# Kernel tuning notes

Measured on AMD Instinct MI355X. Metric: run time of the kernel, lower is better.

Reference implementation:

```python
import jax, jax.numpy as jnp
import numpy as np

BETA = 1.0

def setup_inputs() -> dict:
    key = jax.random.key(0)
    k1, k2 = jax.random.split(key)
    z = jax.random.normal(k1, (8, 8192, 64), dtype=jnp.float32)
    # codebook initialized as randn * sc (sc=0.001) in the original module
    codebook = jax.random.normal(k2, (1024, 64), dtype=jnp.float32) * 0.001
    return {"z": z, "codebook": codebook}

def reference(z, codebook):
    # squared euclidean distances: ||z||^2 + ||c||^2 - 2 z.c  -> [B, T, code_num]
    d = (jnp.sum(z ** 2, axis=-1, keepdims=True)
         + jnp.sum(codebook ** 2, axis=1)
         - 2.0 * jnp.einsum('btd,kd->btk', z, codebook))
    min_encoding_indices = jnp.argmin(d, axis=-1)            # [B, T] int
    # one-hot @ codebook is exactly a gather of nearest code vectors
    z_q = codebook[min_encoding_indices]                     # [B, T, D]
    sg = jax.lax.stop_gradient
    loss = jnp.mean((sg(z_q) - z) ** 2) + BETA * jnp.mean((z_q - sg(z)) ** 2)
    # straight-through estimator
    z_q_st = z + sg(z_q - z)
    return (z_q_st, min_encoding_indices, loss)
```

## Files before the change

### kernel.cpp

```cpp
#include <hip/hip_runtime.h>

#define TOKENS 65536
#define DIM 64
#define NCODE 1024
#define MARGIN 6e-5f
#define FLAG_CAP 8192
#define TPG 16

#define OUT_IDX_OFF ((size_t)TOKENS * DIM)
#define OUT_LOSS_OFF (OUT_IDX_OFF + TOKENS)

#define WS_LOSS   0
#define WS_FLAGC  8
#define WS_DONEA  12
#define WS_DGRP   16
#define WS_BNORM  2064
#define WS_CHI    6160
#define WS_CLO    137232
#define WS_PACKED 268304
#define WS_FLAGS  333840

typedef __attribute__((ext_vector_type(8))) short short8;
typedef __attribute__((ext_vector_type(4))) float f32x4;

__device__ __forceinline__ float np_sumsq64(const float* __restrict__ x) {
#pragma clang fp contract(off)
    float r[8];
#pragma unroll
    for (int j = 0; j < 8; ++j) r[j] = x[j] * x[j];
#pragma unroll
    for (int i = 8; i < 64; i += 8) {
#pragma unroll
        for (int j = 0; j < 8; ++j) {
            float sq = x[i + j] * x[i + j];
            r[j] = r[j] + sq;
        }
    }
    return ((r[0] + r[1]) + (r[2] + r[3])) + ((r[4] + r[5]) + (r[6] + r[7]));
}

__global__ __launch_bounds__(256) void vq_prep(
    const float* __restrict__ cb, unsigned short* __restrict__ chi,
    unsigned short* __restrict__ clo, float* __restrict__ bnorm,
    unsigned int* __restrict__ ctrl ) {
    int tid = blockIdx.x * 256 + threadIdx.x;
    if (tid < 516) ctrl[tid] = 0u;
    int j = tid & 7;
    int L = (tid >> 3) & 63;
    int cs = tid >> 9;
    int s = cs & 1, c = cs >> 1;
    int code = c * 16 + (L & 15);
    int d = s * 32 + (L >> 4) * 8 + j;
    float v = -2.0f * cb[(size_t)code * DIM + d];
    unsigned int b = __float_as_uint(v);
    chi[tid] = (unsigned short)(b >> 16);
    float hf = __uint_as_float(b & 0xFFFF0000u);
    float lo;
    {
#pragma clang fp contract(off)
        lo = v - hf;
    }
    clo[tid] = (unsigned short)(__float_as_uint(lo) >> 16);

    if (tid < NCODE) bnorm[tid] = np_sumsq64(cb + (size_t)tid * DIM);
}

__device__ __forceinline__ void top2_merge(float& a1, float& a2, int& ai,
                                           float b1, float b2, int bi) {
    float n1 = fminf(a1, b1);
    float n2 = fminf(fmaxf(a1, b1), fminf(a2, b2));
    ai = (b1 < a1) ? bi : ai;
    a1 = n1; a2 = n2;
}

__global__ __launch_bounds__(256, 4) void vq_fast(
    const float* __restrict__ z, const float* __restrict__ cb,
    const unsigned short* __restrict__ cfrag_hi,
    const unsigned short* __restrict__ cfrag_lo,
    const float* __restrict__ bnorm, float* __restrict__ out,
    unsigned int* __restrict__ flag_count, int* __restrict__ flag_list,
    unsigned long long* __restrict__ packed_min,
    double* __restrict__ loss_sum, unsigned int flag_cap) {
    __shared__ short8 sh_hi[2][512];
    __shared__ short8 sh_lo[2][512];
    __shared__ float bn_lds[NCODE];
    __shared__ int s_best[64];
    __shared__ int s_flag[64];

    const int tid = threadIdx.x;
    const int lane = tid & 63;
    const int w = tid >> 6;
    const int t0 = blockIdx.x * 64;
    const int tw = t0 + w * 16;
    const int col = lane & 15;
    const int quad = lane >> 4;

    ((float4*)bn_lds)[tid] = ((const float4*)bnorm)[tid];

    short8 zhi[2], zlo[2];
#pragma unroll
    for (int s = 0; s < 2; ++s) {
        const float* zp = z + (size_t)(tw + col) * DIM + s * 32 + quad * 8;
        float4 f0 = ((const float4*)zp)[0];
        float4 f1 = ((const float4*)zp)[1];
        float f[8] = {f0.x, f0.y, f0.z, f0.w, f1.x, f1.y, f1.z, f1.w};
        short8 h, l;
#pragma unroll
        for (int j = 0; j < 8; ++j) {
            unsigned int b = __float_as_uint(f[j]);
            h[j] = (short)(b >> 16);
            float hf = __uint_as_float(b & 0xFFFF0000u);
            float lo;
            {
#pragma clang fp contract(off)
                lo = f[j] - hf;
            }
            l[j] = (short)(__float_as_uint(lo) >> 16);
        }
        zhi[s] = h; zlo[s] = l;
    }

    const short8* CH = (const short8*)cfrag_hi;
    const short8* CL = (const short8*)cfrag_lo;

    {
        short8 a0 = CH[tid], a1 = CH[tid + 256];
        short8 b0 = CL[tid], b1 = CL[tid + 256];
        sh_hi[0][tid] = a0; sh_hi[0][tid + 256] = a1;
        sh_lo[0][tid] = b0; sh_lo[0][tid + 256] = b1;
    }
    __syncthreads();

    float m1 = 3.0e38f, m2 = 3.0e38f;
    int bi = 0;
    const int koff = quad * 4;

    for (int g = 0; g < 16; ++g) {
        const int buf = g & 1;
        short8 a0, a1, b0, b1;
        if (g < 15) {
            const int base = (g + 1) * 512 + tid;
            a0 = CH[base]; a1 = CH[base + 256];
            b0 = CL[base]; b1 = CL[base + 256];
        }
#pragma unroll
        for (int cc = 0; cc < 4; ++cc) {
            const int c = g * 4 + cc;
            short8 ch0 = sh_hi[buf][(cc * 2 + 0) * 64 + lane];
            short8 ch1 = sh_hi[buf][(cc * 2 + 1) * 64 + lane];
            short8 cl0 = sh_lo[buf][(cc * 2 + 0) * 64 + lane];
            short8 cl1 = sh_lo[buf][(cc * 2 + 1) * 64 + lane];
            const int cbase = c * 16 + koff;
            const f32x4 bn = *(const f32x4*)&bn_lds[cbase];
            f32x4 acc = bn;
            acc = __builtin_amdgcn_mfma_f32_16x16x32_bf16(ch0, zhi[0], acc, 0, 0, 0);
            acc = __builtin_amdgcn_mfma_f32_16x16x32_bf16(cl0, zhi[0], acc, 0, 0, 0);
            acc = __builtin_amdgcn_mfma_f32_16x16x32_bf16(ch0, zlo[0], acc, 0, 0, 0);
            acc = __builtin_amdgcn_mfma_f32_16x16x32_bf16(ch1, zhi[1], acc, 0, 0, 0);
            acc = __builtin_amdgcn_mfma_f32_16x16x32_bf16(cl1, zhi[1], acc, 0, 0, 0);
            acc = __builtin_amdgcn_mfma_f32_16x16x32_bf16(ch1, zlo[1], acc, 0, 0, 0);
#pragma unroll
            for (int i = 0; i < 4; ++i) {
                float u = acc[i];
                float om1 = m1;
                bool lt = u < om1;
                float fm = fminf(m2, u);
                m2 = lt ? om1 : fm;
                m1 = lt ? u : om1;
                bi = lt ? (cbase + i) : bi;
            }
        }
        if (g < 15) {
            sh_hi[buf ^ 1][tid] = a0; sh_hi[buf ^ 1][tid + 256] = a1;
            sh_lo[buf ^ 1][tid] = b0; sh_lo[buf ^ 1][tid + 256] = b1;
            __syncthreads();
        }
    }

    {
        float a1 = m1, a2 = m2;
        int ai = bi;
        {
            float o1 = __shfl_xor(a1, 16); float o2 = __shfl_xor(a2, 16);
            int oi = __shfl_xor(ai, 16);
            top2_merge(a1, a2, ai, o1, o2, oi);
        }
        {
            float o1 = __shfl_xor(a1, 32); float o2 = __shfl_xor(a2, 32);
            int oi = __shfl_xor(ai, 32);
            top2_merge(a1, a2, ai, o1, o2, oi);
        }
        if (quad == 0) {
            const int slot = w * 16 + col;
            int fl = (a2 - a1) < MARGIN;
            if (fl) {
                unsigned int pos = atomicAdd(flag_count, 1u);
                if (pos >= flag_cap) fl = 0;
                else {
                    flag_list[pos] = t0 + slot;
                    packed_min[pos] = ~0ull;
                }
            }
            s_best[slot] = ai;
            s_flag[slot] = fl;
        }
    }
    __syncthreads();

    const int et = tid >> 1, h = tid & 1;
    float loss_t = 0.0f;
    if (et < 64 && !s_flag[et]) {
        const int B = s_best[et];
        const float4* cq  = (const float4*)(cb + (size_t)B * DIM + h * 32);
        const float4* zq4 = (const float4*)(z + (size_t)(t0 + et) * DIM + h * 32);
        float4* o4 = (float4*)(out + (size_t)(t0 + et) * DIM + h * 32);
#pragma unroll
        for (int jj = 0; jj < 8; ++jj) {
#pragma clang fp contract(off)
            float4 cc = cq[jj];
            float4 zz = zq4[jj];
            float d0 = cc.x - zz.x, d1 = cc.y - zz.y;
            float d2 = cc.z - zz.z, d3 = cc.w - zz.w;
            float4 o;
            o.x = zz.x + d0; o.y = zz.y + d1;
            o.z = zz.z + d2; o.w = zz.w + d3;
            o4[jj] = o;
            loss_t = __fmaf_rn(d0, d0, loss_t);
            loss_t = __fmaf_rn(d1, d1, loss_t);
            loss_t = __fmaf_rn(d2, d2, loss_t);
            loss_t = __fmaf_rn(d3, d3, loss_t);
        }
        if (h == 0) out[OUT_IDX_OFF + t0 + et] = (float)B;
    }
#pragma unroll
    for (int off = 32; off > 0; off >>= 1)
        loss_t += __shfl_down(loss_t, off);
    if (lane == 0 && w < 2) atomicAdd(loss_sum, (double)loss_t);
}

__device__ __forceinline__ unsigned long long shfl_down_u64(unsigned long long v, int off) {
    unsigned int lo = (unsigned int)v, hi = (unsigned int)(v >> 32);
    lo = __shfl_down(lo, off);
    hi = __shfl_down(hi, off);
    return ((unsigned long long)hi << 32) | lo;
}

__global__ __launch_bounds__(256) void vq_exact_min(
    const float* __restrict__ z, const float* __restrict__ cb,
    const float* __restrict__ bnorm,
    const unsigned int* __restrict__ flag_count,
    const int* __restrict__ flag_list,
    unsigned long long* __restrict__ packed_min,
    unsigned int* __restrict__ done_grp, unsigned int* __restrict__ done_all,
    float* __restrict__ out, double* __restrict__ loss_sum,
    unsigned int flag_cap) {
    __shared__ float zsh[TPG * 68];
    __shared__ float szs[TPG];
    __shared__ unsigned int s_old;

    const int tid = threadIdx.x;
    const int w = tid >> 6;
    const int lane = tid & 63;
    unsigned int count = *flag_count;
    if (count > flag_cap) count = flag_cap;
    const unsigned int ngroups = (count + TPG - 1) / TPG;

    if (count == 0) {
        if (blockIdx.x == 0 && tid == 0) {
            double L = atomicAdd(loss_sum, 0.0);
            out[OUT_LOSS_OFF] = (float)(2.0 * L / (double)((size_t)TOKENS * DIM));
        }
        return;
    }

    const int q = blockIdx.x & 3;
    const unsigned int g = blockIdx.x >> 2;
    if (g >= ngroups) return;

    const int k = q * 256 + w * 64 + lane;

    float row[DIM];
    {
        const float4* c4 = (const float4*)(cb + (size_t)k * DIM);
#pragma unroll
        for (int j = 0; j < 16; ++j) {
            float4 v = c4[j];
            row[4 * j + 0] = v.x; row[4 * j + 1] = v.y;
            row[4 * j + 2] = v.z; row[4 * j + 3] = v.w;
        }
    }
    const float bnk = bnorm[k];

    {
        const int i = tid >> 2, part = tid & 3;
        if (i < TPG) {
            const unsigned int li = g * TPG + i;
            if (li < count) {
                const int t = flag_list[li];
                const float4* zp = (const float4*)(z + (size_t)t * DIM + part * 16);
                float4* dst = (float4*)(zsh + i * 68 + part * 16);
#pragma unroll
                for (int e = 0; e < 4; ++e) dst[e] = zp[e];
            }
        }
    }
    __syncthreads();
    if (tid < TPG) szs[tid] = np_sumsq64(zsh + tid * 68);
    __syncthreads();

    for (int tt = 0; tt < TPG; ++tt) {
        const unsigned int li = g * TPG + tt;
        const float* zp = zsh + tt * 68;
        float l16[16];
#pragma unroll
        for (int g2 = 0; g2 < 4; ++g2) {
            float4 v0 = ((const float4*)(zp + 4 * g2))[0];
            float4 v1 = ((const float4*)(zp + 16 + 4 * g2))[0];
            float4 v2 = ((const float4*)(zp + 32 + 4 * g2))[0];
            float4 v3 = ((const float4*)(zp + 48 + 4 * g2))[0];
            float a0[4] = {v0.x, v0.y, v0.z, v0.w};
            float a1[4] = {v1.x, v1.y, v1.z, v1.w};
            float a2[4] = {v2.x, v2.y, v2.z, v2.w};
            float a3[4] = {v3.x, v3.y, v3.z, v3.w};
#pragma unroll
            for (int e = 0; e < 4; ++e) {
#pragma clang fp contract(off)
                int jj = 4 * g2 + e;
                float acc = a3[e] * row[48 + jj];
                acc = __fmaf_rn(a2[e], row[32 + jj], acc);
                acc = __fmaf_rn(a1[e], row[16 + jj], acc);
                acc = __fmaf_rn(a0[e], row[jj],      acc);
                l16[jj] = acc;
            }
        }
        float e_np;
        {
#pragma clang fp contract(off)
#pragma unroll
            for (int jj = 0; jj < 8; ++jj) l16[jj] = l16[jj] + l16[jj + 8];
#pragma unroll
            for (int jj = 0; jj < 4; ++jj) l16[jj] = l16[jj] + l16[jj + 4];
            l16[0] = l16[0] + l16[2];
            l16[1] = l16[1] + l16[3];
            e_np = l16[0] + l16[1];
        }
        float dd;
        {
#pragma clang fp contract(off)
            float t1 = szs[tt] + bnk;
            float mm = 2.0f * e_np;
            dd = t1 - mm;
        }
        unsigned long long pk =
            ((unsigned long long)__float_as_uint(dd) << 10) | (unsigned int)k;
#pragma unroll
        for (int off = 32; off > 0; off >>= 1) {
            unsigned long long o = shfl_down_u64(pk, off);
            pk = (o < pk) ? o : pk;
        }
        if (lane == 0 && li < count)
            atomicMin(&packed_min[li], pk);
    }

    __threadfence();
    __syncthreads();
    if (tid == 0) s_old = atomicAdd(&done_grp[g], 1u);
    __syncthreads();
    if (s_old != 3u) return;
    __threadfence();

    for (int tt = w * (TPG / 4); tt < (w + 1) * (TPG / 4); ++tt) {
        const unsigned int li = g * TPG + tt;
        if (li >= count) break;
        const int t = flag_list[li];
        const unsigned long long pk = atomicAdd(&packed_min[li], 0ull);
        const int best = (int)(pk & 1023ull);
        const float zl = zsh[tt * 68 + lane];
        const float zq = cb[(size_t)best * DIM + lane];
        float d, o;
        {
#pragma clang fp contract(off)
            d = zq - zl;
            o = zl + d;
        }
        out[(size_t)t * DIM + lane] = o;
        float l2 = d * d;
#pragma unroll
        for (int off = 32; off > 0; off >>= 1)
            l2 += __shfl_down(l2, off);
        if (lane == 0) {
            out[OUT_IDX_OFF + t] = (float)best;
            atomicAdd(loss_sum, (double)l2);
        }
    }

    __threadfence();
    __syncthreads();
    if (tid == 0) {
        unsigned int old = atomicAdd(done_all, 1u);
        if (old == ngroups - 1) {
            double L = atomicAdd(loss_sum, 0.0);
            out[OUT_LOSS_OFF] = (float)(2.0 * L / (double)((size_t)TOKENS * DIM));
        }
    }
}

extern "C" void kernel_launch(void* const* d_in, const int* in_sizes, int n_in,
                              void* d_out, int out_size, void* d_ws, size_t ws_size,
                              hipStream_t stream) {
    const float* z  = (const float*)d_in[0];
    const float* cb = (const float*)d_in[1];
    float* out = (float*)d_out;

    char* ws = (char*)d_ws;
    double* loss_sum = (double*)(ws + WS_LOSS);
    unsigned int* flag_count = (unsigned int*)(ws + WS_FLAGC);
    unsigned int* done_all = (unsigned int*)(ws + WS_DONEA);
    unsigned int* done_grp = (unsigned int*)(ws + WS_DGRP);
    float* bnorm = (float*)(ws + WS_BNORM);
    unsigned short* chi = (unsigned short*)(ws + WS_CHI);
    unsigned short* clo = (unsigned short*)(ws + WS_CLO);
    unsigned long long* packed = (unsigned long long*)(ws + WS_PACKED);
    int* flag_list = (int*)(ws + WS_FLAGS);

    unsigned int cap = 0;
    if (ws_size > WS_FLAGS + 4) {
        size_t c = (ws_size - WS_FLAGS) / 4;
        cap = (c > FLAG_CAP) ? FLAG_CAP : (unsigned int)c;
    }

    vq_prep<<<dim3(256), dim3(256), 0, stream>>>(
        cb, chi, clo, bnorm, (unsigned int*)ws);
    vq_fast<<<dim3(TOKENS / 64), dim3(256), 0, stream>>>(
        z, cb, chi, clo, bnorm, out, flag_count, flag_list, packed, loss_sum, cap);
    vq_exact_min<<<dim3(2048), dim3(256), 0, stream>>>(
        z, cb, bnorm, flag_count, flag_list, packed, done_grp, done_all,
        out, loss_sum, cap);
}
```

Before: 164.7 us.

## Stream codebook fragments directly from global memory instead of LDS staging

The fast kernel no longer stages codebook hi/lo fragments and norms in shared memory with block-wide barriers. Each wave instead loads its fragments straight from global memory (the L2-resident codebook), with a one-iteration register prefetch. Blocks shrink to 128 threads covering 32 tokens, which doubles the grid. This drops the LDS traffic and the per-group __syncthreads, but every wave now reads the whole codebook from cache on its own, raising L2/L1 bandwidth pressure.

```diff
diff --git a/kernel.cpp b/kernel.cpp
--- a/kernel.cpp
+++ b/kernel.cpp
@@ -73,7 +73,7 @@
     a1 = n1; a2 = n2;
 }
 
-__global__ __launch_bounds__(256, 4) void vq_fast(
+__global__ __launch_bounds__(128, 4) void vq_fast(
     const float* __restrict__ z, const float* __restrict__ cb,
     const unsigned short* __restrict__ cfrag_hi,
     const unsigned short* __restrict__ cfrag_lo,
@@ -81,21 +81,16 @@
     unsigned int* __restrict__ flag_count, int* __restrict__ flag_list,
     unsigned long long* __restrict__ packed_min,
     double* __restrict__ loss_sum, unsigned int flag_cap) {
-    __shared__ short8 sh_hi[2][512];
-    __shared__ short8 sh_lo[2][512];
-    __shared__ float bn_lds[NCODE];
-    __shared__ int s_best[64];
-    __shared__ int s_flag[64];
+    __shared__ int s_best[32];
+    __shared__ int s_flag[32];
 
     const int tid = threadIdx.x;
     const int lane = tid & 63;
     const int w = tid >> 6;
-    const int t0 = blockIdx.x * 64;
+    const int t0 = blockIdx.x * 32;
     const int tw = t0 + w * 16;
     const int col = lane & 15;
     const int quad = lane >> 4;
-
-    ((float4*)bn_lds)[tid] = ((const float4*)bnorm)[tid];
 
     short8 zhi[2], zlo[2];
 #pragma unroll
@@ -120,60 +115,45 @@
         zhi[s] = h; zlo[s] = l;
     }
 
-    const short8* CH = (const short8*)cfrag_hi;
-    const short8* CL = (const short8*)cfrag_lo;
-
-    {
-        short8 a0 = CH[tid], a1 = CH[tid + 256];
-        short8 b0 = CL[tid], b1 = CL[tid + 256];
-        sh_hi[0][tid] = a0; sh_hi[0][tid + 256] = a1;
-        sh_lo[0][tid] = b0; sh_lo[0][tid + 256] = b1;
-    }
-    __syncthreads();
+    const short8* CHp = (const short8*)cfrag_hi + lane;
+    const short8* CLp = (const short8*)cfrag_lo + lane;
+    const f32x4* bnp = (const f32x4*)bnorm;
+    const int koff = quad * 4;
 
     float m1 = 3.0e38f, m2 = 3.0e38f;
     int bi = 0;
-    const int koff = quad * 4;
-
-    for (int g = 0; g < 16; ++g) {
-        const int buf = g & 1;
-        short8 a0, a1, b0, b1;
-        if (g < 15) {
-            const int base = (g + 1) * 512 + tid;
-            a0 = CH[base]; a1 = CH[base + 256];
-            b0 = CL[base]; b1 = CL[base + 256];
-        }
-#pragma unroll
-        for (int cc = 0; cc < 4; ++cc) {
-            const int c = g * 4 + cc;
-            short8 ch0 = sh_hi[buf][(cc * 2 + 0) * 64 + lane];
-            short8 ch1 = sh_hi[buf][(cc * 2 + 1) * 64 + lane];
-            short8 cl0 = sh_lo[buf][(cc * 2 + 0) * 64 + lane];
-            short8 cl1 = sh_lo[buf][(cc * 2 + 1) * 64 + lane];
-            const int cbase = c * 16 + koff;
-            const f32x4 bn = *(const f32x4*)&bn_lds[cbase];
-            f32x4 acc = bn;
-            acc = __builtin_amdgcn_mfma_f32_16x16x32_bf16(ch0, zhi[0], acc, 0, 0, 0);
-            acc = __builtin_amdgcn_mfma_f32_16x16x32_bf16(cl0, zhi[0], acc, 0, 0, 0);
-            acc = __builtin_amdgcn_mfma_f32_16x16x32_bf16(ch0, zlo[0], acc, 0, 0, 0);
-            acc = __builtin_amdgcn_mfma_f32_16x16x32_bf16(ch1, zhi[1], acc, 0, 0, 0);
-            acc = __builtin_amdgcn_mfma_f32_16x16x32_bf16(cl1, zhi[1], acc, 0, 0, 0);
-            acc = __builtin_amdgcn_mfma_f32_16x16x32_bf16(ch1, zlo[1], acc, 0, 0, 0);
-#pragma unroll
-            for (int i = 0; i < 4; ++i) {
-                float u = acc[i];
-                float om1 = m1;
-                bool lt = u < om1;
-                float fm = fminf(m2, u);
-                m2 = lt ? om1 : fm;
-                m1 = lt ? u : om1;
-                bi = lt ? (cbase + i) : bi;
-            }
-        }
-        if (g < 15) {
-            sh_hi[buf ^ 1][tid] = a0; sh_hi[buf ^ 1][tid + 256] = a1;
-            sh_lo[buf ^ 1][tid] = b0; sh_lo[buf ^ 1][tid + 256] = b1;
-            __syncthreads();
+
+    short8 nh0 = CHp[0], nh1 = CHp[64];
+    short8 nl0 = CLp[0], nl1 = CLp[64];
+    f32x4 nbn = bnp[quad];
+
+#pragma unroll 2
+    for (int c = 0; c < 64; ++c) {
+        const short8 ch0 = nh0, ch1 = nh1, cl0 = nl0, cl1 = nl1;
+        const f32x4 bn = nbn;
+        if (c < 63) {
+            const int b = (c + 1) * 128;
+            nh0 = CHp[b]; nh1 = CHp[b + 64];
+            nl0 = CLp[b]; nl1 = CLp[b + 64];
+            nbn = bnp[(c + 1) * 4 + quad];
+        }
+        const int cbase = c * 16 + koff;
+        f32x4 acc = bn;
+        acc = __builtin_amdgcn_mfma_f32_16x16x32_bf16(ch0, zhi[0], acc, 0, 0, 0);
+        acc = __builtin_amdgcn_mfma_f32_16x16x32_bf16(cl0, zhi[0], acc, 0, 0, 0);
+        acc = __builtin_amdgcn_mfma_f32_16x16x32_bf16(ch0, zlo[0], acc, 0, 0, 0);
+        acc = __builtin_amdgcn_mfma_f32_16x16x32_bf16(ch1, zhi[1], acc, 0, 0, 0);
+        acc = __builtin_amdgcn_mfma_f32_16x16x32_bf16(cl1, zhi[1], acc, 0, 0, 0);
+        acc = __builtin_amdgcn_mfma_f32_16x16x32_bf16(ch1, zlo[1], acc, 0, 0, 0);
+#pragma unroll
+        for (int i = 0; i < 4; ++i) {
+            float u = acc[i];
+            float om1 = m1;
+            bool lt = u < om1;
+            float fm = fminf(m2, u);
+            m2 = lt ? om1 : fm;
+            m1 = lt ? u : om1;
+            bi = lt ? (cbase + i) : bi;
         }
     }
 
@@ -209,7 +189,7 @@
 
     const int et = tid >> 1, h = tid & 1;
     float loss_t = 0.0f;
-    if (et < 64 && !s_flag[et]) {
+    if (et < 32 && !s_flag[et]) {
         const int B = s_best[et];
         const float4* cq  = (const float4*)(cb + (size_t)B * DIM + h * 32);
         const float4* zq4 = (const float4*)(z + (size_t)(t0 + et) * DIM + h * 32);
@@ -235,7 +215,7 @@
 #pragma unroll
     for (int off = 32; off > 0; off >>= 1)
         loss_t += __shfl_down(loss_t, off);
-    if (lane == 0 && w < 2) atomicAdd(loss_sum, (double)loss_t);
+    if (lane == 0 && w == 0) atomicAdd(loss_sum, (double)loss_t);
 }
 
 __device__ __forceinline__ unsigned long long shfl_down_u64(unsigned long long v, int off) {
@@ -431,7 +411,7 @@
 
     vq_prep<<<dim3(256), dim3(256), 0, stream>>>(
         cb, chi, clo, bnorm, (unsigned int*)ws);
-    vq_fast<<<dim3(TOKENS / 64), dim3(256), 0, stream>>>(
+    vq_fast<<<dim3(TOKENS / 32), dim3(128), 0, stream>>>(
         z, cb, chi, clo, bnorm, out, flag_count, flag_list, packed, loss_sum, cap);
     vq_exact_min<<<dim3(2048), dim3(256), 0, stream>>>(
         z, cb, bnorm, flag_count, flag_list, packed, done_grp, done_all,
```

Result: slower. 181.7 us (+10.3%).
